# Kernel optimization log

Hardware: AMD Instinct MI355X
Metric: run time of the kernel (lower is better)

## Reference

```python
import jax, jax.numpy as jnp
import numpy as np

B, T, C, H = 16, 1024, 768, 64

def setup_inputs() -> dict:
    key = jax.random.key(0)
    ks = jax.random.split(key, 4)
    s = 1.0 / np.sqrt(C)
    return {
        "x": jax.random.normal(ks[0], (B, T, C), dtype=jnp.float32),
        "Wq": jax.random.normal(ks[1], (C, H), dtype=jnp.float32) * s,
        "bq": jnp.zeros((H,), dtype=jnp.float32),
        "Wk": jax.random.normal(ks[2], (C, H), dtype=jnp.float32) * s,
        "bk": jnp.zeros((H,), dtype=jnp.float32),
        "Wv": jax.random.normal(ks[3], (C, H), dtype=jnp.float32) * s,
        "bv": jnp.zeros((H,), dtype=jnp.float32),
    }

def reference(x, Wq, bq, Wk, bk, Wv, bv):
    # single-head causal attention (dropout = eval/identity)
    q = x @ Wq + bq          # [B,T,H]
    k = x @ Wk + bk          # [B,T,H]
    v = x @ Wv + bv          # [B,T,H]
    scale = 1.0 / jnp.sqrt(jnp.asarray(q.shape[-1], q.dtype))
    wei = jnp.einsum("bth,bsh->bts", q, k) * scale  # [B,T,T]
    causal = jnp.tril(jnp.ones((q.shape[1], q.shape[1]), dtype=bool))
    wei = jnp.where(causal, wei, -jnp.inf)
    wei = jax.nn.softmax(wei, axis=-1)
    out = jnp.einsum("bts,bsh->bth", wei, v)        # [B,T,H]
    return out
```

## Files before the change

### kernel.cpp

```cpp
#include <hip/hip_runtime.h>
#include <hip/hip_bf16.h>
#include <math.h>

#define B_ 16
#define T_ 1024
#define C_ 768
#define H_ 64

typedef __attribute__((ext_vector_type(8))) short bf16x8;
typedef __attribute__((ext_vector_type(4))) float f32x4;

__device__ __forceinline__ short f2bf(float f) {
  union { float f; unsigned u; } un;
  un.f = f;
  unsigned r = un.u + 0x7FFFu + ((un.u >> 16) & 1u);
  return (short)(r >> 16);
}

__global__ __launch_bounds__(256) void prep_w(
    const float* __restrict__ Wq, const float* __restrict__ Wk,
    const float* __restrict__ Wv, short* __restrict__ wfrag) {
  const int o = blockIdx.x * 256 + threadIdx.x;
  const int j = o & 7;
  const int l = (o >> 3) & 63;
  const int fid = o >> 9;
  const int ct = fid % 12;
  const int ks = fid / 12;
  const int mat = ct >> 2;
  const int col = (ct & 3) * 16 + (l & 15);
  const int k = ks * 32 + (l >> 4) * 8 + j;
  const float* W = (mat == 0) ? Wq : (mat == 1) ? Wk : Wv;
  wfrag[o] = f2bf(W[(size_t)k * H_ + col]);
}

#define QKV_LDSF 6400

__global__ __launch_bounds__(128, 2) void qkv_gemm(
    const float* __restrict__ x, const short* __restrict__ wfrag,
    const float* __restrict__ bq, const float* __restrict__ bk,
    const float* __restrict__ bv, short* __restrict__ qkv) {
  __shared__ float lds[QKV_LDSF];
  const int rt = blockIdx.x;
  const int w  = threadIdx.x >> 6;
  const int l  = threadIdx.x & 63;
  const int lo = l & 15, hi = l >> 4;
  const int kh = w;

  float* stg = lds + w * 3072;
  const char* xb = (const char*)(x + (size_t)rt * 16 * C_ + kh * 384);

  auto STAGE = [&](int buf, int c) {
    #pragma unroll
    for (int s = 0; s < 4; ++s) {
      const int r = s * 4 + hi;
      const char* src = xb + (size_t)r * (C_ * 4) + (size_t)c * 256
                        + ((lo * 16) ^ ((r & 7) << 4));
      float* dst = stg + buf * 1024 + s * 256;
      __builtin_amdgcn_global_load_lds(
          (const __attribute__((address_space(1))) void*)src,
          (__attribute__((address_space(3))) void*)dst, 16, 0, 0);
    }
  };

  f32x4 acc[12];
  #pragma unroll
  for (int ct = 0; ct < 12; ++ct) acc[ct] = (f32x4){0.f, 0.f, 0.f, 0.f};

  STAGE(0, 0);
  STAGE(1, 1);

  #pragma unroll
  for (int c = 0; c < 6; ++c) {
    const int buf = c % 3;
    __builtin_amdgcn_sched_barrier(0);
    bf16x8 wf0[12], wf1[12];
    const int ksb = kh * 12 + c * 2;
    #pragma unroll
    for (int ct = 0; ct < 12; ++ct) {
      wf0[ct] = *(const bf16x8*)(wfrag + ((size_t)(ksb * 12 + ct) << 9) + l * 8);
      wf1[ct] = *(const bf16x8*)(wfrag + ((size_t)((ksb + 1) * 12 + ct) << 9) + l * 8);
    }
    __builtin_amdgcn_sched_barrier(0);
    if (c < 4) STAGE((c + 2) % 3, c + 2);
    __builtin_amdgcn_sched_barrier(0);
    if (c < 4)      { asm volatile("s_waitcnt vmcnt(32)" ::: "memory"); }
    else if (c < 5) { asm volatile("s_waitcnt vmcnt(28)" ::: "memory"); }
    else            { asm volatile("s_waitcnt vmcnt(24)" ::: "memory"); }
    __builtin_amdgcn_sched_barrier(0);
    bf16x8 af0, af1;
    {
      const char* rp = (const char*)(stg + buf * 1024) + lo * 256;
      const int sw = (lo & 7) << 4;
      f32x4 x0 = *(const f32x4*)(rp + ((hi * 32)       ^ sw));
      f32x4 x1 = *(const f32x4*)(rp + ((hi * 32 + 16)  ^ sw));
      f32x4 x2 = *(const f32x4*)(rp + ((128 + hi * 32)      ^ sw));
      f32x4 x3 = *(const f32x4*)(rp + ((128 + hi * 32 + 16) ^ sw));
      #pragma unroll
      for (int j = 0; j < 4; ++j) {
        af0[j] = f2bf(x0[j]); af0[4 + j] = f2bf(x1[j]);
        af1[j] = f2bf(x2[j]); af1[4 + j] = f2bf(x3[j]);
      }
    }
    __builtin_amdgcn_s_setprio(1);
    #pragma unroll
    for (int ct = 0; ct < 12; ++ct)
      acc[ct] = __builtin_amdgcn_mfma_f32_16x16x32_bf16(af0, wf0[ct], acc[ct], 0, 0, 0);
    #pragma unroll
    for (int ct = 0; ct < 12; ++ct)
      acc[ct] = __builtin_amdgcn_mfma_f32_16x16x32_bf16(af1, wf1[ct], acc[ct], 0, 0, 0);
    __builtin_amdgcn_s_setprio(0);
  }

  __syncthreads();
  #pragma unroll
  for (int ct = 0; ct < 12; ++ct)
    #pragma unroll
    for (int r = 0; r < 4; ++r)
      lds[w * 3136 + (hi * 4 + r) * 196 + ct * 16 + lo] = acc[ct][r];
  __syncthreads();

  {
    const int row = threadIdx.x >> 3;
    const int c0 = (threadIdx.x & 7) * 24;
    bf16x8 o0, o1, o2;
    #pragma unroll
    for (int j = 0; j < 24; ++j) {
      const int col = c0 + j;
      float s = lds[row * 196 + col] + lds[3136 + row * 196 + col];
      const int mat = col >> 6;
      const float* bb = (mat == 0) ? bq : (mat == 1) ? bk : bv;
      s += bb[col & 63];
      const short v = f2bf(s);
      if (j < 8) o0[j] = v; else if (j < 16) o1[j - 8] = v; else o2[j - 16] = v;
    }
    short* op = qkv + ((size_t)(rt * 16 + row)) * 192 + c0;
    *(bf16x8*)(op)      = o0;
    *(bf16x8*)(op + 8)  = o1;
    *(bf16x8*)(op + 16) = o2;
  }
}

__global__ __launch_bounds__(256) void vtrans(const short* __restrict__ qkv,
                                              short* __restrict__ vt) {
  __shared__ short tile[64][66];
  const int b = blockIdx.y;
  const int tb = blockIdx.x * 64;
  const int tid = threadIdx.x;

  {
    const int tt = tid >> 2, c = (tid & 3) * 16;
    const short* src = qkv + (size_t)(b * T_ + tb + tt) * 192 + 128 + c;
    bf16x8 v0 = *(const bf16x8*)(src);
    bf16x8 v1 = *(const bf16x8*)(src + 8);
    #pragma unroll
    for (int j = 0; j < 8; ++j) { tile[tt][c + j] = v0[j]; tile[tt][c + 8 + j] = v1[j]; }
  }
  __syncthreads();
  {
    const int n = tid >> 2, toff = (tid & 3) * 16;
    short* dst = vt + ((size_t)(b * H_ + n)) * T_ + tb + toff;
    bf16x8 o0, o1;
    #pragma unroll
    for (int j = 0; j < 8; ++j) { o0[j] = tile[toff + j][n]; o1[j] = tile[toff + 8 + j][n]; }
    *(bf16x8*)(dst) = o0;
    *(bf16x8*)(dst + 8) = o1;
  }
}

#define SCALE_LOG2E 0.18033688011114382f

__global__ __launch_bounds__(256) void flash(
    const short* __restrict__ qkv, const short* __restrict__ vt,
    float* __restrict__ out) {
  __shared__ __align__(16) short p_lds[4][16][72];
  __shared__ float o_sh[4][16][64];
  __shared__ float ml_sh[4][2][16];

  const int wgid = blockIdx.x;
  const int kk = wgid >> 3;
  const int qt = 63 - (kk & 63);
  const int b  = (wgid & 7) + 8 * (kk >> 6);

  const int w = threadIdx.x >> 6;
  const int l = threadIdx.x & 63;
  const int lo = l & 15, hi = l >> 4;

  const int dtile = qt >> 2;
  const int ntot = dtile + 1;
  const int span = (ntot + 3) >> 2;
  const int kv0 = w * span;
  const int kv1 = min(ntot, kv0 + span);
  const int qr = qt & 3;

  const short* qrow = qkv + (size_t)(b * T_ + qt * 16 + lo) * 192;
  bf16x8 qf0 = *(const bf16x8*)(qrow + hi * 8);
  bf16x8 qf1 = *(const bf16x8*)(qrow + 32 + hi * 8);

  float m_l = -1e30f;
  float l_l = 0.f;
  f32x4 oacc[4];
  #pragma unroll
  for (int dt = 0; dt < 4; ++dt) oacc[dt] = (f32x4){0.f, 0.f, 0.f, 0.f};

  for (int kvt = kv0; kvt < kv1; ++kvt) {
    const bool diag = (kvt == dtile);
    const int nct = diag ? (qr + 1) : 4;

    bf16x8 kf[8], vf[8];
    #pragma unroll
    for (int ct = 0; ct < 4; ++ct) {
      const short* krow = qkv + (size_t)(b * T_ + kvt * 64 + ct * 16 + lo) * 192 + 64;
      kf[2 * ct]     = *(const bf16x8*)(krow + hi * 8);
      kf[2 * ct + 1] = *(const bf16x8*)(krow + 32 + hi * 8);
    }
    #pragma unroll
    for (int dt = 0; dt < 4; ++dt) {
      const short* vrow = vt + (size_t)(b * H_ + dt * 16 + lo) * T_ + kvt * 64;
      vf[2 * dt]     = *(const bf16x8*)(vrow + hi * 8);
      vf[2 * dt + 1] = *(const bf16x8*)(vrow + 32 + hi * 8);
    }

    f32x4 sv[4];
    #pragma unroll
    for (int ct = 0; ct < 4; ++ct) sv[ct] = (f32x4){0.f, 0.f, 0.f, 0.f};
    __builtin_amdgcn_s_setprio(1);
    #pragma unroll
    for (int ct = 0; ct < 4; ++ct) {
      if (ct < nct) {
        sv[ct] = __builtin_amdgcn_mfma_f32_16x16x32_bf16(kf[2 * ct], qf0, sv[ct], 0, 0, 0);
        sv[ct] = __builtin_amdgcn_mfma_f32_16x16x32_bf16(kf[2 * ct + 1], qf1, sv[ct], 0, 0, 0);
      }
    }
    __builtin_amdgcn_s_setprio(0);

    #pragma unroll
    for (int ct = 0; ct < 4; ++ct) {
      #pragma unroll
      for (int r = 0; r < 4; ++r) {
        float s = (ct < nct) ? sv[ct][r] * SCALE_LOG2E : -1e30f;
        if (diag && ct == qr && (hi * 4 + r) > lo) s = -1e30f;
        sv[ct][r] = s;
      }
    }

    float tmax = sv[0][0];
    #pragma unroll
    for (int ct = 0; ct < 4; ++ct)
      #pragma unroll
      for (int r = 0; r < 4; ++r) tmax = fmaxf(tmax, sv[ct][r]);
    tmax = fmaxf(tmax, __shfl_xor(tmax, 16));
    tmax = fmaxf(tmax, __shfl_xor(tmax, 32));
    const float mn = fmaxf(m_l, tmax);
    const float corr = exp2f(m_l - mn);
    m_l = mn;
    float psum = 0.f;
    #pragma unroll
    for (int ct = 0; ct < 4; ++ct) {
      #pragma unroll
      for (int r = 0; r < 4; ++r) {
        float p = exp2f(sv[ct][r] - mn);
        sv[ct][r] = p;
        psum += p;
      }
    }
    psum += __shfl_xor(psum, 16);
    psum += __shfl_xor(psum, 32);
    l_l = l_l * corr + psum;

    #pragma unroll
    for (int ct = 0; ct < 4; ++ct) {
      __hip_bfloat162 p01 = __float22bfloat162_rn(float2{sv[ct][0], sv[ct][1]});
      __hip_bfloat162 p23 = __float22bfloat162_rn(float2{sv[ct][2], sv[ct][3]});
      uint2 pk;
      pk.x = *reinterpret_cast<unsigned*>(&p01);
      pk.y = *reinterpret_cast<unsigned*>(&p23);
      *reinterpret_cast<uint2*>(&p_lds[w][lo][ct * 16 + hi * 4]) = pk;
    }

    #pragma unroll
    for (int r = 0; r < 4; ++r) {
      const float cr = __shfl(corr, hi * 4 + r);
      #pragma unroll
      for (int dt = 0; dt < 4; ++dt) oacc[dt][r] *= cr;
    }

    bf16x8 pa0 = *(const bf16x8*)(&p_lds[w][lo][hi * 8]);
    bf16x8 pa1 = *(const bf16x8*)(&p_lds[w][lo][32 + hi * 8]);
    __builtin_amdgcn_s_setprio(1);
    #pragma unroll
    for (int dt = 0; dt < 4; ++dt) {
      oacc[dt] = __builtin_amdgcn_mfma_f32_16x16x32_bf16(pa0, vf[2 * dt], oacc[dt], 0, 0, 0);
      oacc[dt] = __builtin_amdgcn_mfma_f32_16x16x32_bf16(pa1, vf[2 * dt + 1], oacc[dt], 0, 0, 0);
    }
    __builtin_amdgcn_s_setprio(0);
  }

  #pragma unroll
  for (int dt = 0; dt < 4; ++dt)
    #pragma unroll
    for (int r = 0; r < 4; ++r)
      o_sh[w][hi * 4 + r][dt * 16 + lo] = oacc[dt][r];
  if (hi == 0) {
    ml_sh[w][0][lo] = m_l;
    ml_sh[w][1][lo] = l_l;
  }
  __syncthreads();

  {
    const int row = threadIdx.x >> 4;
    const int c0 = (threadIdx.x & 15) * 4;
    float M = fmaxf(fmaxf(ml_sh[0][0][row], ml_sh[1][0][row]),
                    fmaxf(ml_sh[2][0][row], ml_sh[3][0][row]));
    float e[4];
    float L = 0.f;
    #pragma unroll
    for (int w2 = 0; w2 < 4; ++w2) {
      e[w2] = exp2f(ml_sh[w2][0][row] - M);
      L += ml_sh[w2][1][row] * e[w2];
    }
    f32x4 o;
    #pragma unroll
    for (int j = 0; j < 4; ++j) {
      float O = 0.f;
      #pragma unroll
      for (int w2 = 0; w2 < 4; ++w2) O += e[w2] * o_sh[w2][row][c0 + j];
      o[j] = O / L;
    }
    *(f32x4*)(out + (size_t)(b * T_ + qt * 16 + row) * H_ + c0) = o;
  }
}

extern "C" void kernel_launch(void* const* d_in, const int* in_sizes, int n_in,
                              void* d_out, int out_size, void* d_ws, size_t ws_size,
                              hipStream_t stream) {
  const float* x  = (const float*)d_in[0];
  const float* Wq = (const float*)d_in[1];
  const float* bq = (const float*)d_in[2];
  const float* Wk = (const float*)d_in[3];
  const float* bk = (const float*)d_in[4];
  const float* Wv = (const float*)d_in[5];
  const float* bv = (const float*)d_in[6];
  float* out = (float*)d_out;

  short* wfrag = (short*)d_ws;
  short* qkv = wfrag + (size_t)3 * H_ * C_;
  short* vtb = qkv + (size_t)B_ * T_ * 192;

  prep_w<<<dim3(576), dim3(256), 0, stream>>>(Wq, Wk, Wv, wfrag);
  qkv_gemm<<<dim3(1024), dim3(128), 0, stream>>>(x, wfrag, bq, bk, bv, qkv);
  vtrans<<<dim3(T_ / 64, B_), dim3(256), 0, stream>>>(qkv, vtb);
  flash<<<dim3(1024), dim3(256), 0, stream>>>(qkv, vtb, out);
}
```

Before: 55.09 us.

## Split QKV GEMM K across four waves with LDS atomic reduction; lazy softmax rescale

The QKV projection kernel now runs 4 waves per block instead of 2. Each wave handles a quarter of the C reduction with a smaller staging buffer, and the partial tiles are combined through LDS float atomicAdd into a zeroed pool. The goal is more waves in flight to hide x load latency, at the cost of LDS atomics, an extra zero-init barrier, and half the threads sitting idle during the epilogue. In the flash kernel, the running max and the rescaling of the output accumulator now update only when some lane's new max exceeds the old one by more than 8 in log2 space. This skips per-tile exp/shuffle/multiply work, but unnormalized exponentials can grow up to 2^8, which risks precision loss or overflow in bf16/fp32.

```diff
diff --git a/kernel.cpp b/kernel.cpp
--- a/kernel.cpp
+++ b/kernel.cpp
@@ -33,29 +33,37 @@
   wfrag[o] = f2bf(W[(size_t)k * H_ + col]);
 }
 
-#define QKV_LDSF 6400
-
-__global__ __launch_bounds__(128, 2) void qkv_gemm(
+#define QKV_LDSF 9280
+
+__global__ __launch_bounds__(256, 3) void qkv_gemm(
     const float* __restrict__ x, const short* __restrict__ wfrag,
     const float* __restrict__ bq, const float* __restrict__ bk,
     const float* __restrict__ bv, short* __restrict__ qkv) {
   __shared__ float lds[QKV_LDSF];
   const int rt = blockIdx.x;
-  const int w  = threadIdx.x >> 6;
-  const int l  = threadIdx.x & 63;
+  const int tid = threadIdx.x;
+  const int w  = tid >> 6;
+  const int l  = tid & 63;
   const int lo = l & 15, hi = l >> 4;
-  const int kh = w;
-
-  float* stg = lds + w * 3072;
-  const char* xb = (const char*)(x + (size_t)rt * 16 * C_ + kh * 384);
+
+  float* pool = lds + 6144;
+  #pragma unroll
+  for (int i = 0; i < 13; ++i) {
+    const int idx = tid + i * 256;
+    if (idx < 3136) pool[idx] = 0.f;
+  }
+  __syncthreads();
+
+  float* stg = lds + w * 1536;
+  const char* xb = (const char*)(x + (size_t)rt * 16 * C_ + w * 192);
 
   auto STAGE = [&](int buf, int c) {
     #pragma unroll
-    for (int s = 0; s < 4; ++s) {
-      const int r = s * 4 + hi;
-      const char* src = xb + (size_t)r * (C_ * 4) + (size_t)c * 256
-                        + ((lo * 16) ^ ((r & 7) << 4));
-      float* dst = stg + buf * 1024 + s * 256;
+    for (int s = 0; s < 2; ++s) {
+      const int row = s * 8 + (l >> 3);
+      const char* src = xb + (size_t)row * (C_ * 4) + (size_t)c * 128
+                        + (((l & 7) * 16) ^ ((row & 7) << 4));
+      float* dst = stg + buf * 512 + s * 256;
       __builtin_amdgcn_global_load_lds(
           (const __attribute__((address_space(1))) void*)src,
           (__attribute__((address_space(3))) void*)dst, 16, 0, 0);
@@ -73,60 +81,51 @@
   for (int c = 0; c < 6; ++c) {
     const int buf = c % 3;
     __builtin_amdgcn_sched_barrier(0);
-    bf16x8 wf0[12], wf1[12];
-    const int ksb = kh * 12 + c * 2;
-    #pragma unroll
-    for (int ct = 0; ct < 12; ++ct) {
-      wf0[ct] = *(const bf16x8*)(wfrag + ((size_t)(ksb * 12 + ct) << 9) + l * 8);
-      wf1[ct] = *(const bf16x8*)(wfrag + ((size_t)((ksb + 1) * 12 + ct) << 9) + l * 8);
-    }
+    bf16x8 wf[12];
+    const int ks = w * 6 + c;
+    #pragma unroll
+    for (int ct = 0; ct < 12; ++ct)
+      wf[ct] = *(const bf16x8*)(wfrag + ((size_t)(ks * 12 + ct) << 9) + l * 8);
     __builtin_amdgcn_sched_barrier(0);
     if (c < 4) STAGE((c + 2) % 3, c + 2);
     __builtin_amdgcn_sched_barrier(0);
-    if (c < 4)      { asm volatile("s_waitcnt vmcnt(32)" ::: "memory"); }
-    else if (c < 5) { asm volatile("s_waitcnt vmcnt(28)" ::: "memory"); }
-    else            { asm volatile("s_waitcnt vmcnt(24)" ::: "memory"); }
+    if (c == 0)      { asm volatile("s_waitcnt vmcnt(16)" ::: "memory"); }
+    else if (c < 4)  { asm volatile("s_waitcnt vmcnt(28)" ::: "memory"); }
+    else if (c == 4) { asm volatile("s_waitcnt vmcnt(26)" ::: "memory"); }
+    else             { asm volatile("s_waitcnt vmcnt(24)" ::: "memory"); }
     __builtin_amdgcn_sched_barrier(0);
-    bf16x8 af0, af1;
+    bf16x8 af;
     {
-      const char* rp = (const char*)(stg + buf * 1024) + lo * 256;
+      const char* rowbase = (const char*)(stg + buf * 512)
+                            + (lo >> 3) * 1024 + (lo & 7) * 128;
       const int sw = (lo & 7) << 4;
-      f32x4 x0 = *(const f32x4*)(rp + ((hi * 32)       ^ sw));
-      f32x4 x1 = *(const f32x4*)(rp + ((hi * 32 + 16)  ^ sw));
-      f32x4 x2 = *(const f32x4*)(rp + ((128 + hi * 32)      ^ sw));
-      f32x4 x3 = *(const f32x4*)(rp + ((128 + hi * 32 + 16) ^ sw));
-      #pragma unroll
-      for (int j = 0; j < 4; ++j) {
-        af0[j] = f2bf(x0[j]); af0[4 + j] = f2bf(x1[j]);
-        af1[j] = f2bf(x2[j]); af1[4 + j] = f2bf(x3[j]);
-      }
+      f32x4 x0 = *(const f32x4*)(rowbase + ((hi * 32)      ^ sw));
+      f32x4 x1 = *(const f32x4*)(rowbase + ((hi * 32 + 16) ^ sw));
+      #pragma unroll
+      for (int j = 0; j < 4; ++j) { af[j] = f2bf(x0[j]); af[4 + j] = f2bf(x1[j]); }
     }
     __builtin_amdgcn_s_setprio(1);
     #pragma unroll
     for (int ct = 0; ct < 12; ++ct)
-      acc[ct] = __builtin_amdgcn_mfma_f32_16x16x32_bf16(af0, wf0[ct], acc[ct], 0, 0, 0);
-    #pragma unroll
-    for (int ct = 0; ct < 12; ++ct)
-      acc[ct] = __builtin_amdgcn_mfma_f32_16x16x32_bf16(af1, wf1[ct], acc[ct], 0, 0, 0);
+      acc[ct] = __builtin_amdgcn_mfma_f32_16x16x32_bf16(af, wf[ct], acc[ct], 0, 0, 0);
     __builtin_amdgcn_s_setprio(0);
   }
 
+  #pragma unroll
+  for (int ct = 0; ct < 12; ++ct)
+    #pragma unroll
+    for (int r = 0; r < 4; ++r)
+      atomicAdd(&pool[(hi * 4 + r) * 196 + ct * 16 + lo], acc[ct][r]);
   __syncthreads();
-  #pragma unroll
-  for (int ct = 0; ct < 12; ++ct)
-    #pragma unroll
-    for (int r = 0; r < 4; ++r)
-      lds[w * 3136 + (hi * 4 + r) * 196 + ct * 16 + lo] = acc[ct][r];
-  __syncthreads();
-
-  {
-    const int row = threadIdx.x >> 3;
-    const int c0 = (threadIdx.x & 7) * 24;
+
+  if (tid < 128) {
+    const int row = tid >> 3;
+    const int c0 = (tid & 7) * 24;
     bf16x8 o0, o1, o2;
     #pragma unroll
     for (int j = 0; j < 24; ++j) {
       const int col = c0 + j;
-      float s = lds[row * 196 + col] + lds[3136 + row * 196 + col];
+      float s = pool[row * 196 + col];
       const int mat = col >> 6;
       const float* bb = (mat == 0) ? bq : (mat == 1) ? bk : bv;
       s += bb[col & 63];
@@ -250,22 +249,33 @@
       for (int r = 0; r < 4; ++r) tmax = fmaxf(tmax, sv[ct][r]);
     tmax = fmaxf(tmax, __shfl_xor(tmax, 16));
     tmax = fmaxf(tmax, __shfl_xor(tmax, 32));
-    const float mn = fmaxf(m_l, tmax);
-    const float corr = exp2f(m_l - mn);
-    m_l = mn;
+
+    if (!__all(tmax - m_l <= 8.0f)) {
+      const float mn = fmaxf(m_l, tmax);
+      const float corr = exp2f(m_l - mn);
+      m_l = mn;
+      l_l *= corr;
+      #pragma unroll
+      for (int r = 0; r < 4; ++r) {
+        const float cr = __shfl(corr, hi * 4 + r);
+        #pragma unroll
+        for (int dt = 0; dt < 4; ++dt) oacc[dt][r] *= cr;
+      }
+    }
+
     float psum = 0.f;
     #pragma unroll
     for (int ct = 0; ct < 4; ++ct) {
       #pragma unroll
       for (int r = 0; r < 4; ++r) {
-        float p = exp2f(sv[ct][r] - mn);
+        float p = exp2f(sv[ct][r] - m_l);
         sv[ct][r] = p;
         psum += p;
       }
     }
     psum += __shfl_xor(psum, 16);
     psum += __shfl_xor(psum, 32);
-    l_l = l_l * corr + psum;
+    l_l += psum;
 
     #pragma unroll
     for (int ct = 0; ct < 4; ++ct) {
@@ -275,13 +285,6 @@
       pk.x = *reinterpret_cast<unsigned*>(&p01);
       pk.y = *reinterpret_cast<unsigned*>(&p23);
       *reinterpret_cast<uint2*>(&p_lds[w][lo][ct * 16 + hi * 4]) = pk;
-    }
-
-    #pragma unroll
-    for (int r = 0; r < 4; ++r) {
-      const float cr = __shfl(corr, hi * 4 + r);
-      #pragma unroll
-      for (int dt = 0; dt < 4; ++dt) oacc[dt][r] *= cr;
     }
 
     bf16x8 pa0 = *(const bf16x8*)(&p_lds[w][lo][hi * 8]);
@@ -347,7 +350,7 @@
   short* vtb = qkv + (size_t)B_ * T_ * 192;
 
   prep_w<<<dim3(576), dim3(256), 0, stream>>>(Wq, Wk, Wv, wfrag);
-  qkv_gemm<<<dim3(1024), dim3(128), 0, stream>>>(x, wfrag, bq, bk, bv, qkv);
+  qkv_gemm<<<dim3(1024), dim3(256), 0, stream>>>(x, wfrag, bq, bk, bv, qkv);
   vtrans<<<dim3(T_ / 64, B_), dim3(256), 0, stream>>>(qkv, vtb);
   flash<<<dim3(1024), dim3(256), 0, stream>>>(qkv, vtb, out);
 }
```

Result: slower. 110.8 us (+101.2%).

## Process two query tiles per flash block and skip small softmax rescales

Applied to the files above, without the earlier changes.

Each flash workgroup now handles two adjacent 16-row query tiles, so every K and V fragment loaded from global memory is used for two sets of MFMAs. The grid shrinks from 1024 to 512 blocks. A lazy-rescale check also skips the running-max update and the accumulator correction unless the new tile max exceeds the old one by more than 8 in log2 units. The trade-offs are higher register pressure, fewer blocks to fill the GPU, and an epilogue that runs twice with extra barriers.

```diff
diff --git a/kernel.cpp b/kernel.cpp
--- a/kernel.cpp
+++ b/kernel.cpp
@@ -172,39 +172,48 @@
 __global__ __launch_bounds__(256) void flash(
     const short* __restrict__ qkv, const short* __restrict__ vt,
     float* __restrict__ out) {
-  __shared__ __align__(16) short p_lds[4][16][72];
+  __shared__ __align__(16) short p_lds[4][2][16][72];
   __shared__ float o_sh[4][16][64];
-  __shared__ float ml_sh[4][2][16];
+  __shared__ float ml_sh[4][2][2][16];
 
   const int wgid = blockIdx.x;
   const int kk = wgid >> 3;
-  const int qt = 63 - (kk & 63);
-  const int b  = (wgid & 7) + 8 * (kk >> 6);
+  const int qp = 31 - (kk & 31);
+  const int b  = (wgid & 7) + 8 * (kk >> 5);
 
   const int w = threadIdx.x >> 6;
   const int l = threadIdx.x & 63;
   const int lo = l & 15, hi = l >> 4;
-
-  const int dtile = qt >> 2;
+  const int off = hi * 4;
+
+  const int qt0 = 2 * qp, qt1 = 2 * qp + 1;
+  const int dtile = qt0 >> 2;
   const int ntot = dtile + 1;
   const int span = (ntot + 3) >> 2;
   const int kv0 = w * span;
   const int kv1 = min(ntot, kv0 + span);
-  const int qr = qt & 3;
-
-  const short* qrow = qkv + (size_t)(b * T_ + qt * 16 + lo) * 192;
-  bf16x8 qf0 = *(const bf16x8*)(qrow + hi * 8);
-  bf16x8 qf1 = *(const bf16x8*)(qrow + 32 + hi * 8);
-
-  float m_l = -1e30f;
-  float l_l = 0.f;
-  f32x4 oacc[4];
-  #pragma unroll
-  for (int dt = 0; dt < 4; ++dt) oacc[dt] = (f32x4){0.f, 0.f, 0.f, 0.f};
+  const int qr0 = qt0 & 3, qr1 = qr0 + 1;
+
+  const short* qrowA = qkv + (size_t)(b * T_ + qt0 * 16 + lo) * 192;
+  bf16x8 qA0 = *(const bf16x8*)(qrowA + hi * 8);
+  bf16x8 qA1 = *(const bf16x8*)(qrowA + 32 + hi * 8);
+  const short* qrowB = qkv + (size_t)(b * T_ + qt1 * 16 + lo) * 192;
+  bf16x8 qB0 = *(const bf16x8*)(qrowB + hi * 8);
+  bf16x8 qB1 = *(const bf16x8*)(qrowB + 32 + hi * 8);
+
+  float mA = -1e30f, lsA = 0.f;
+  float mB = -1e30f, lsB = 0.f;
+  f32x4 oA[4], oB[4];
+  #pragma unroll
+  for (int dt = 0; dt < 4; ++dt) {
+    oA[dt] = (f32x4){0.f, 0.f, 0.f, 0.f};
+    oB[dt] = (f32x4){0.f, 0.f, 0.f, 0.f};
+  }
 
   for (int kvt = kv0; kvt < kv1; ++kvt) {
     const bool diag = (kvt == dtile);
-    const int nct = diag ? (qr + 1) : 4;
+    const int nctA = diag ? (qr0 + 1) : 4;
+    const int nctB = diag ? (qr1 + 1) : 4;
 
     bf16x8 kf[8], vf[8];
     #pragma unroll
@@ -220,15 +229,22 @@
       vf[2 * dt + 1] = *(const bf16x8*)(vrow + 32 + hi * 8);
     }
 
-    f32x4 sv[4];
-    #pragma unroll
-    for (int ct = 0; ct < 4; ++ct) sv[ct] = (f32x4){0.f, 0.f, 0.f, 0.f};
+    f32x4 svA[4], svB[4];
+    #pragma unroll
+    for (int ct = 0; ct < 4; ++ct) {
+      svA[ct] = (f32x4){0.f, 0.f, 0.f, 0.f};
+      svB[ct] = (f32x4){0.f, 0.f, 0.f, 0.f};
+    }
     __builtin_amdgcn_s_setprio(1);
     #pragma unroll
     for (int ct = 0; ct < 4; ++ct) {
-      if (ct < nct) {
-        sv[ct] = __builtin_amdgcn_mfma_f32_16x16x32_bf16(kf[2 * ct], qf0, sv[ct], 0, 0, 0);
-        sv[ct] = __builtin_amdgcn_mfma_f32_16x16x32_bf16(kf[2 * ct + 1], qf1, sv[ct], 0, 0, 0);
+      if (ct < nctA) {
+        svA[ct] = __builtin_amdgcn_mfma_f32_16x16x32_bf16(kf[2 * ct], qA0, svA[ct], 0, 0, 0);
+        svA[ct] = __builtin_amdgcn_mfma_f32_16x16x32_bf16(kf[2 * ct + 1], qA1, svA[ct], 0, 0, 0);
+      }
+      if (ct < nctB) {
+        svB[ct] = __builtin_amdgcn_mfma_f32_16x16x32_bf16(kf[2 * ct], qB0, svB[ct], 0, 0, 0);
+        svB[ct] = __builtin_amdgcn_mfma_f32_16x16x32_bf16(kf[2 * ct + 1], qB1, svB[ct], 0, 0, 0);
       }
     }
     __builtin_amdgcn_s_setprio(0);
@@ -237,86 +253,139 @@
     for (int ct = 0; ct < 4; ++ct) {
       #pragma unroll
       for (int r = 0; r < 4; ++r) {
-        float s = (ct < nct) ? sv[ct][r] * SCALE_LOG2E : -1e30f;
-        if (diag && ct == qr && (hi * 4 + r) > lo) s = -1e30f;
-        sv[ct][r] = s;
-      }
-    }
-
-    float tmax = sv[0][0];
-    #pragma unroll
-    for (int ct = 0; ct < 4; ++ct)
-      #pragma unroll
-      for (int r = 0; r < 4; ++r) tmax = fmaxf(tmax, sv[ct][r]);
-    tmax = fmaxf(tmax, __shfl_xor(tmax, 16));
-    tmax = fmaxf(tmax, __shfl_xor(tmax, 32));
-    const float mn = fmaxf(m_l, tmax);
-    const float corr = exp2f(m_l - mn);
-    m_l = mn;
-    float psum = 0.f;
-    #pragma unroll
-    for (int ct = 0; ct < 4; ++ct) {
-      #pragma unroll
-      for (int r = 0; r < 4; ++r) {
-        float p = exp2f(sv[ct][r] - mn);
-        sv[ct][r] = p;
-        psum += p;
-      }
-    }
-    psum += __shfl_xor(psum, 16);
-    psum += __shfl_xor(psum, 32);
-    l_l = l_l * corr + psum;
-
-    #pragma unroll
-    for (int ct = 0; ct < 4; ++ct) {
-      __hip_bfloat162 p01 = __float22bfloat162_rn(float2{sv[ct][0], sv[ct][1]});
-      __hip_bfloat162 p23 = __float22bfloat162_rn(float2{sv[ct][2], sv[ct][3]});
-      uint2 pk;
-      pk.x = *reinterpret_cast<unsigned*>(&p01);
-      pk.y = *reinterpret_cast<unsigned*>(&p23);
-      *reinterpret_cast<uint2*>(&p_lds[w][lo][ct * 16 + hi * 4]) = pk;
-    }
-
-    #pragma unroll
-    for (int r = 0; r < 4; ++r) {
-      const float cr = __shfl(corr, hi * 4 + r);
-      #pragma unroll
-      for (int dt = 0; dt < 4; ++dt) oacc[dt][r] *= cr;
-    }
-
-    bf16x8 pa0 = *(const bf16x8*)(&p_lds[w][lo][hi * 8]);
-    bf16x8 pa1 = *(const bf16x8*)(&p_lds[w][lo][32 + hi * 8]);
+        float sA = (ct < nctA) ? svA[ct][r] * SCALE_LOG2E : -1e30f;
+        if (diag && ct == qr0 && (off + r) > lo) sA = -1e30f;
+        svA[ct][r] = sA;
+        float sB = (ct < nctB) ? svB[ct][r] * SCALE_LOG2E : -1e30f;
+        if (diag && ct == qr1 && (off + r) > lo) sB = -1e30f;
+        svB[ct][r] = sB;
+      }
+    }
+
+    {
+      float tmax = svA[0][0];
+      #pragma unroll
+      for (int ct = 0; ct < 4; ++ct)
+        #pragma unroll
+        for (int r = 0; r < 4; ++r) tmax = fmaxf(tmax, svA[ct][r]);
+      tmax = fmaxf(tmax, __shfl_xor(tmax, 16));
+      tmax = fmaxf(tmax, __shfl_xor(tmax, 32));
+      if (!__all(tmax - mA <= 8.0f)) {
+        const float mn = fmaxf(mA, tmax);
+        const float corr = exp2f(mA - mn);
+        mA = mn;
+        lsA *= corr;
+        #pragma unroll
+        for (int r = 0; r < 4; ++r) {
+          const float cr = __shfl(corr, off + r);
+          #pragma unroll
+          for (int dt = 0; dt < 4; ++dt) oA[dt][r] *= cr;
+        }
+      }
+      float psum = 0.f;
+      #pragma unroll
+      for (int ct = 0; ct < 4; ++ct) {
+        #pragma unroll
+        for (int r = 0; r < 4; ++r) {
+          float p = exp2f(svA[ct][r] - mA);
+          svA[ct][r] = p;
+          psum += p;
+        }
+      }
+      psum += __shfl_xor(psum, 16);
+      psum += __shfl_xor(psum, 32);
+      lsA += psum;
+      #pragma unroll
+      for (int ct = 0; ct < 4; ++ct) {
+        __hip_bfloat162 p01 = __float22bfloat162_rn(float2{svA[ct][0], svA[ct][1]});
+        __hip_bfloat162 p23 = __float22bfloat162_rn(float2{svA[ct][2], svA[ct][3]});
+        uint2 pk;
+        pk.x = *reinterpret_cast<unsigned*>(&p01);
+        pk.y = *reinterpret_cast<unsigned*>(&p23);
+        *reinterpret_cast<uint2*>(&p_lds[w][0][lo][ct * 16 + off]) = pk;
+      }
+    }
+    {
+      float tmax = svB[0][0];
+      #pragma unroll
+      for (int ct = 0; ct < 4; ++ct)
+        #pragma unroll
+        for (int r = 0; r < 4; ++r) tmax = fmaxf(tmax, svB[ct][r]);
+      tmax = fmaxf(tmax, __shfl_xor(tmax, 16));
+      tmax = fmaxf(tmax, __shfl_xor(tmax, 32));
+      if (!__all(tmax - mB <= 8.0f)) {
+        const float mn = fmaxf(mB, tmax);
+        const float corr = exp2f(mB - mn);
+        mB = mn;
+        lsB *= corr;
+        #pragma unroll
+        for (int r = 0; r < 4; ++r) {
+          const float cr = __shfl(corr, off + r);
+          #pragma unroll
+          for (int dt = 0; dt < 4; ++dt) oB[dt][r] *= cr;
+        }
+      }
+      float psum = 0.f;
+      #pragma unroll
+      for (int ct = 0; ct < 4; ++ct) {
+        #pragma unroll
+        for (int r = 0; r < 4; ++r) {
+          float p = exp2f(svB[ct][r] - mB);
+          svB[ct][r] = p;
+          psum += p;
+        }
+      }
+      psum += __shfl_xor(psum, 16);
+      psum += __shfl_xor(psum, 32);
+      lsB += psum;
+      #pragma unroll
+      for (int ct = 0; ct < 4; ++ct) {
+        __hip_bfloat162 p01 = __float22bfloat162_rn(float2{svB[ct][0], svB[ct][1]});
+        __hip_bfloat162 p23 = __float22bfloat162_rn(float2{svB[ct][2], svB[ct][3]});
+        uint2 pk;
+        pk.x = *reinterpret_cast<unsigned*>(&p01);
+        pk.y = *reinterpret_cast<unsigned*>(&p23);
+        *reinterpret_cast<uint2*>(&p_lds[w][1][lo][ct * 16 + off]) = pk;
+      }
+    }
+
+    bf16x8 paA0 = *(const bf16x8*)(&p_lds[w][0][lo][hi * 8]);
+    bf16x8 paA1 = *(const bf16x8*)(&p_lds[w][0][lo][32 + hi * 8]);
+    bf16x8 paB0 = *(const bf16x8*)(&p_lds[w][1][lo][hi * 8]);
+    bf16x8 paB1 = *(const bf16x8*)(&p_lds[w][1][lo][32 + hi * 8]);
     __builtin_amdgcn_s_setprio(1);
     #pragma unroll
     for (int dt = 0; dt < 4; ++dt) {
-      oacc[dt] = __builtin_amdgcn_mfma_f32_16x16x32_bf16(pa0, vf[2 * dt], oacc[dt], 0, 0, 0);
-      oacc[dt] = __builtin_amdgcn_mfma_f32_16x16x32_bf16(pa1, vf[2 * dt + 1], oacc[dt], 0, 0, 0);
+      oA[dt] = __builtin_amdgcn_mfma_f32_16x16x32_bf16(paA0, vf[2 * dt], oA[dt], 0, 0, 0);
+      oA[dt] = __builtin_amdgcn_mfma_f32_16x16x32_bf16(paA1, vf[2 * dt + 1], oA[dt], 0, 0, 0);
+      oB[dt] = __builtin_amdgcn_mfma_f32_16x16x32_bf16(paB0, vf[2 * dt], oB[dt], 0, 0, 0);
+      oB[dt] = __builtin_amdgcn_mfma_f32_16x16x32_bf16(paB1, vf[2 * dt + 1], oB[dt], 0, 0, 0);
     }
     __builtin_amdgcn_s_setprio(0);
   }
 
+  if (hi == 0) {
+    ml_sh[w][0][0][lo] = mA;  ml_sh[w][0][1][lo] = lsA;
+    ml_sh[w][1][0][lo] = mB;  ml_sh[w][1][1][lo] = lsB;
+  }
+
   #pragma unroll
   for (int dt = 0; dt < 4; ++dt)
     #pragma unroll
     for (int r = 0; r < 4; ++r)
-      o_sh[w][hi * 4 + r][dt * 16 + lo] = oacc[dt][r];
-  if (hi == 0) {
-    ml_sh[w][0][lo] = m_l;
-    ml_sh[w][1][lo] = l_l;
-  }
-  __syncthreads();
-
+      o_sh[w][off + r][dt * 16 + lo] = oA[dt][r];
+  __syncthreads();
   {
     const int row = threadIdx.x >> 4;
     const int c0 = (threadIdx.x & 15) * 4;
-    float M = fmaxf(fmaxf(ml_sh[0][0][row], ml_sh[1][0][row]),
-                    fmaxf(ml_sh[2][0][row], ml_sh[3][0][row]));
+    float M = fmaxf(fmaxf(ml_sh[0][0][0][row], ml_sh[1][0][0][row]),
+                    fmaxf(ml_sh[2][0][0][row], ml_sh[3][0][0][row]));
     float e[4];
     float L = 0.f;
     #pragma unroll
     for (int w2 = 0; w2 < 4; ++w2) {
-      e[w2] = exp2f(ml_sh[w2][0][row] - M);
-      L += ml_sh[w2][1][row] * e[w2];
+      e[w2] = exp2f(ml_sh[w2][0][0][row] - M);
+      L += ml_sh[w2][0][1][row] * e[w2];
     }
     f32x4 o;
     #pragma unroll
@@ -326,7 +395,36 @@
       for (int w2 = 0; w2 < 4; ++w2) O += e[w2] * o_sh[w2][row][c0 + j];
       o[j] = O / L;
     }
-    *(f32x4*)(out + (size_t)(b * T_ + qt * 16 + row) * H_ + c0) = o;
+    *(f32x4*)(out + (size_t)(b * T_ + qt0 * 16 + row) * H_ + c0) = o;
+  }
+  __syncthreads();
+  #pragma unroll
+  for (int dt = 0; dt < 4; ++dt)
+    #pragma unroll
+    for (int r = 0; r < 4; ++r)
+      o_sh[w][off + r][dt * 16 + lo] = oB[dt][r];
+  __syncthreads();
+  {
+    const int row = threadIdx.x >> 4;
+    const int c0 = (threadIdx.x & 15) * 4;
+    float M = fmaxf(fmaxf(ml_sh[0][1][0][row], ml_sh[1][1][0][row]),
+                    fmaxf(ml_sh[2][1][0][row], ml_sh[3][1][0][row]));
+    float e[4];
+    float L = 0.f;
+    #pragma unroll
+    for (int w2 = 0; w2 < 4; ++w2) {
+      e[w2] = exp2f(ml_sh[w2][1][0][row] - M);
+      L += ml_sh[w2][1][1][row] * e[w2];
+    }
+    f32x4 o;
+    #pragma unroll
+    for (int j = 0; j < 4; ++j) {
+      float O = 0.f;
+      #pragma unroll
+      for (int w2 = 0; w2 < 4; ++w2) O += e[w2] * o_sh[w2][row][c0 + j];
+      o[j] = O / L;
+    }
+    *(f32x4*)(out + (size_t)(b * T_ + qt1 * 16 + row) * H_ + c0) = o;
   }
 }
 
@@ -349,5 +447,5 @@
   prep_w<<<dim3(576), dim3(256), 0, stream>>>(Wq, Wk, Wv, wfrag);
   qkv_gemm<<<dim3(1024), dim3(128), 0, stream>>>(x, wfrag, bq, bk, bv, qkv);
   vtrans<<<dim3(T_ / 64, B_), dim3(256), 0, stream>>>(qkv, vtb);
-  flash<<<dim3(1024), dim3(256), 0, stream>>>(qkv, vtb, out);
-}
+  flash<<<dim3(512), dim3(256), 0, stream>>>(qkv, vtb, out);
+}
```

Measured after the change: 51.85 us. 1.06x faster.
